# Optimization experiments

Measured on AMD Instinct MI355X. Metric: run time of the kernel, lower is better.

## Reference

```python
import jax, jax.numpy as jnp
import numpy as np

HEADS = 16
DIM_HEAD = 64
QUERY_DIM = 1024
INNER_DIM = HEADS * DIM_HEAD  # 1024
SCALE = DIM_HEAD ** (-0.5)


def setup_inputs() -> dict:
    key = jax.random.key(0)
    ks = jax.random.split(key, 6)
    B, S = 4, 2048
    hidden_states = jax.random.normal(ks[0], (B, S, QUERY_DIM), dtype=jnp.float32)
    # Linear weights stored as [in, out] for x @ W convention
    init = 1.0 / np.sqrt(QUERY_DIM)
    Wq = jax.random.uniform(ks[1], (QUERY_DIM, INNER_DIM), jnp.float32, -init, init)
    Wk = jax.random.uniform(ks[2], (QUERY_DIM, INNER_DIM), jnp.float32, -init, init)
    Wv = jax.random.uniform(ks[3], (QUERY_DIM, INNER_DIM), jnp.float32, -init, init)
    Wo = jax.random.uniform(ks[4], (INNER_DIM, QUERY_DIM), jnp.float32, -init, init)
    bo = jax.random.uniform(ks[5], (QUERY_DIM,), jnp.float32, -init, init)
    return {"hidden_states": hidden_states, "Wq": Wq, "Wk": Wk, "Wv": Wv, "Wo": Wo, "bo": bo}


def reference(hidden_states, Wq, Wk, Wv, Wo, bo):
    B, S, _ = hidden_states.shape
    # Projections
    q = hidden_states @ Wq  # [B,S,inner]
    k = hidden_states @ Wk
    v = hidden_states @ Wv
    # [B, H, S, D]
    q = q.reshape(B, S, HEADS, DIM_HEAD).transpose(0, 2, 1, 3)
    k = k.reshape(B, S, HEADS, DIM_HEAD).transpose(0, 2, 1, 3)
    v = v.reshape(B, S, HEADS, DIM_HEAD).transpose(0, 2, 1, 3)
    # Attention scores and softmax (scale after matmul, as in source)
    scores = jnp.einsum('bhqd,bhkd->bhqk', q, k) * SCALE
    attn = jax.nn.softmax(scores, axis=-1)
    out = jnp.einsum('bhqk,bhkd->bhqd', attn, v)  # [B,H,S,D]
    out = out.transpose(0, 2, 1, 3).reshape(B, S, INNER_DIM)
    return out @ Wo + bo
```

## Files before the change

kernel.cpp:

```cpp
#include <hip/hip_runtime.h>
#include <stdint.h>

typedef short v8s __attribute__((ext_vector_type(8)));
typedef float v4f __attribute__((ext_vector_type(4)));
typedef unsigned int u32;
typedef unsigned short us;

#define LOG2E 1.44269504088896340736f

__device__ __forceinline__ u32 f2u(float x) {
  union { float f; u32 u; } t; t.f = x; return t.u;
}

__device__ __forceinline__ unsigned short bfr(float x) {
  u32 u = f2u(x);
  u32 r = u + 0x7FFFu + ((u >> 16) & 1u);
  return (unsigned short)(r >> 16);
}

__device__ __forceinline__ u32 pk2(float a, float b) {
  return __builtin_amdgcn_perm(f2u(b) + 0x8000u, f2u(a) + 0x8000u, 0x07060302u);
}

__device__ __forceinline__ void async16(const void* g, void* l) {
  __builtin_amdgcn_global_load_lds(
      (const __attribute__((address_space(1))) u32*)g,
      (__attribute__((address_space(3))) u32*)l, 16, 0, 0);
}

#define MFMA_K32(A, B, C) __builtin_amdgcn_mfma_f32_16x16x32_bf16((A), (B), (C), 0, 0, 0)

__global__ void cast_h_kernel(const float4* __restrict__ in, ushort4* __restrict__ out, int n4) {
  int i = blockIdx.x * blockDim.x + threadIdx.x;
  if (i < n4) {
    float4 v = in[i];
    ushort4 o;
    o.x = bfr(v.x); o.y = bfr(v.y); o.z = bfr(v.z); o.w = bfr(v.w);
    out[i] = o;
  }
}

__global__ void transpose_cast4_kernel(const float* __restrict__ W0, const float* __restrict__ W1,
                                       const float* __restrict__ W2, const float* __restrict__ W3,
                                       us* __restrict__ O0, us* __restrict__ O1,
                                       us* __restrict__ O2, us* __restrict__ O3) {
  __shared__ float tile[32][33];
  const int z = blockIdx.z;
  const float* in = (z == 0) ? W0 : (z == 1) ? W1 : (z == 2) ? W2 : W3;
  us* out = (z == 0) ? O0 : (z == 1) ? O1 : (z == 2) ? O2 : O3;
  const float scale = (z == 0) ? 0.125f * LOG2E : 1.0f;
  const int N = 1024;
  int n0 = blockIdx.x * 32, k0 = blockIdx.y * 32;
  int tx = threadIdx.x, ty = threadIdx.y;
#pragma unroll
  for (int j = 0; j < 32; j += 8)
    tile[ty + j][tx] = in[(size_t)(k0 + ty + j) * N + n0 + tx];
  __syncthreads();
#pragma unroll
  for (int j = 0; j < 32; j += 8)
    out[(size_t)(n0 + ty + j) * 1024 + k0 + tx] = bfr(tile[tx][ty + j] * scale);
}

template <int MODE>
__global__ __launch_bounds__(512, 2)
void gemm3_kernel(const us* __restrict__ A, const us* __restrict__ Bt,
                  us* __restrict__ dQ, us* __restrict__ dK, us* __restrict__ dV,
                  float* __restrict__ outF, const float* __restrict__ bias) {
  __shared__ __align__(16) us sm[73728];
  us* const AsB = sm;
  us* const BsB = sm + 3 * 8192;

  const int tid = threadIdx.x;
  const int wid = tid >> 6;
  const int lane = tid & 63;
  const int quad = lane >> 4;
  const int l16 = lane & 15;
  const int tile_m = blockIdx.y * 128;
  const int tile_n = blockIdx.x * 256;
  const bool vpath = (MODE == 3) && (tile_n >= 2048);

  const int srow = tid >> 3;
  const int sc = tid & 7;
  const int scg = sc ^ (srow & 7);

  const us* const GA = A + (size_t)(tile_m + srow) * 1024 + scg * 8;
  const us* const GB = Bt + (size_t)(tile_n + srow) * 1024 + scg * 8;
  us* const LA = AsB + srow * 64 + sc * 8;
  us* const LB = BsB + srow * 64 + sc * 8;

  auto ISSUE = [&](int j, int b) {
    const us* ga = GA + j * 64;
    us* la = LA + b * 8192;
#pragma unroll
    for (int it = 0; it < 2; ++it)
      async16(ga + it * 64 * 1024, la + it * 64 * 64);
    const us* gb = GB + j * 64;
    us* lb = LB + b * 16384;
#pragma unroll
    for (int it = 0; it < 4; ++it)
      async16(gb + it * 64 * 1024, lb + it * 64 * 64);
  };

  v4f zero = {0.f, 0.f, 0.f, 0.f};
  v4f acc[4][4];
#pragma unroll
  for (int i = 0; i < 4; ++i)
#pragma unroll
    for (int j = 0; j < 4; ++j) acc[i][j] = zero;

  const int wm = (wid >> 2) * 64;
  const int wn = (wid & 3) * 64;

  ISSUE(0, 0);
  ISSUE(1, 1);

  int bt = 0;
#pragma unroll 1
  for (int t = 0; t < 16; ++t) {
    if (t < 15)
      asm volatile("s_waitcnt vmcnt(6)" ::: "memory");
    else
      asm volatile("s_waitcnt vmcnt(0)" ::: "memory");
    __builtin_amdgcn_s_barrier();
    asm volatile("" ::: "memory");

    if (t + 2 < 16) {
      int b2 = bt + 2;
      if (b2 >= 3) b2 -= 3;
      ISSUE(t + 2, b2);
    }

    const us* As = AsB + bt * 8192;
    const us* Bs = BsB + bt * 16384;
#pragma unroll
    for (int ks = 0; ks < 2; ++ks) {
      v8s a[4], b[4];
#pragma unroll
      for (int i = 0; i < 4; ++i) {
        int row = wm + i * 16 + l16;
        a[i] = *(const v8s*)&As[row * 64 + (((ks * 4 + quad) ^ (row & 7)) * 8)];
      }
#pragma unroll
      for (int j = 0; j < 4; ++j) {
        int row = wn + j * 16 + l16;
        b[j] = *(const v8s*)&Bs[row * 64 + (((ks * 4 + quad) ^ (row & 7)) * 8)];
      }
      __builtin_amdgcn_s_setprio(1);
      if (vpath) {
#pragma unroll
        for (int i = 0; i < 4; ++i)
#pragma unroll
          for (int j = 0; j < 4; ++j)
            acc[i][j] = MFMA_K32(a[i], b[j], acc[i][j]);
      } else {
#pragma unroll
        for (int i = 0; i < 4; ++i)
#pragma unroll
          for (int j = 0; j < 4; ++j)
            acc[i][j] = MFMA_K32(b[j], a[i], acc[i][j]);
      }
      __builtin_amdgcn_s_setprio(0);
    }
    if (++bt >= 3) bt = 0;
  }

  if (MODE == 2) {
#pragma unroll
    for (int i = 0; i < 4; ++i) {
      int row = tile_m + wm + i * 16 + l16;
#pragma unroll
      for (int j = 0; j < 4; ++j) {
        int col = tile_n + wn + j * 16 + quad * 4;
        float4 bv = *(const float4*)&bias[col];
        float4 o;
        o.x = acc[i][j][0] + bv.x; o.y = acc[i][j][1] + bv.y;
        o.z = acc[i][j][2] + bv.z; o.w = acc[i][j][3] + bv.w;
        *(float4*)&outF[(size_t)row * 1024 + col] = o;
      }
    }
  } else if (!vpath) {
    us* base = (tile_n < 1024) ? dQ : dK;
    const int coln = tile_n & 1023;
#pragma unroll
    for (int i = 0; i < 4; ++i) {
      int row = tile_m + wm + i * 16 + l16;
      int b_ = row >> 11, s_ = row & 2047;
#pragma unroll
      for (int j = 0; j < 4; ++j) {
        int col = coln + wn + j * 16 + quad * 4;
        int h = (col >> 6) & 15, d = col & 63;
        uint2 pk = make_uint2(pk2(acc[i][j][0], acc[i][j][1]), pk2(acc[i][j][2], acc[i][j][3]));
        *(uint2*)&base[((size_t)(b_ * 16 + h) * 2048 + s_) * 64 + d] = pk;
      }
    }
  } else {
    __syncthreads();
    const int vn = tile_n - 2048;
#pragma unroll
    for (int i = 0; i < 4; ++i) {
      int sp = wm + (i >> 1) * 32 + quad * 8 + (i & 1) * 4;
#pragma unroll
      for (int j = 0; j < 4; ++j) {
        int col = wn + j * 16 + l16;
        uint2 pk = make_uint2(pk2(acc[i][j][0], acc[i][j][1]), pk2(acc[i][j][2], acc[i][j][3]));
        *(uint2*)&sm[col * 132 + sp] = pk;
      }
    }
    __syncthreads();
    const int b_ = tile_m >> 11;
    const int sbase = tile_m & 2047;
#pragma unroll
    for (int it = 0; it < 8; ++it) {
      int u = it * 512 + tid;
      int col = u >> 4, sp = (u & 15) * 8;
      v8s val = *(const v8s*)&sm[col * 132 + sp];
      int colg = vn + col;
      int h = (colg >> 6) & 15, d = colg & 63;
      *(v8s*)&dV[((size_t)(b_ * 16 + h) * 64 + d) * 2048 + sbase + sp] = val;
    }
  }
}

__global__ __launch_bounds__(256, 2)
void flash_kernel(const us* __restrict__ Q, const us* __restrict__ K,
                  const us* __restrict__ Vt, us* __restrict__ O) {
  __shared__ __align__(16) us sm[16384];
  us* Ks = sm;
  us* Vts = sm + 8192;

  const int tid = threadIdx.x;
  const int wid = tid >> 6;
  const int lane = tid & 63;
  const int quad = lane >> 4;
  const int l16 = lane & 15;
  const int id = blockIdx.x;
  const int bh = id & 63;
  const int q0 = (id >> 6) * 256;
  const int wq = wid * 64;
  const us* Qp = Q + (size_t)bh * (2048 * 64);
  const us* Kp = K + (size_t)bh * (2048 * 64);
  const us* Vp = Vt + (size_t)bh * (64 * 2048);

  v8s qB[4][2];
#pragma unroll
  for (int mi = 0; mi < 4; ++mi)
#pragma unroll
    for (int ks = 0; ks < 2; ++ks)
      qB[mi][ks] = *(const v8s*)&Qp[(size_t)(q0 + wq + mi * 16 + l16) * 64 + ks * 32 + quad * 8];

  v4f zero = {0.f, 0.f, 0.f, 0.f};
  v4f o[4][4];
#pragma unroll
  for (int i = 0; i < 4; ++i)
#pragma unroll
    for (int mi = 0; mi < 4; ++mi) o[i][mi] = zero;
  v4f l_acc[4] = {zero, zero, zero, zero};
  const us one_bf = 0x3F80;
  const v8s ones = {(short)one_bf, (short)one_bf, (short)one_bf, (short)one_bf,
                    (short)one_bf, (short)one_bf, (short)one_bf, (short)one_bf};

  for (int kv0 = 0; kv0 < 2048; kv0 += 128) {
    __syncthreads();
    {
      int r0 = wid * 32 + (lane >> 3);
      int c = lane & 7;
#pragma unroll
      for (int it = 0; it < 4; ++it) {
        int rr = r0 + it * 8;
        int cg = c ^ (rr & 7);
        async16(Kp + (size_t)(kv0 + rr) * 64 + cg * 8, &Ks[rr * 64 + c * 8]);
      }
    }
    {
      int d0 = wid * 16 + (lane >> 4);
      int c = lane & 15;
#pragma unroll
      for (int it = 0; it < 4; ++it) {
        int dd = d0 + it * 4;
        int cg = c ^ (dd & 15);
        async16(Vp + (size_t)dd * 2048 + kv0 + cg * 8, &Vts[dd * 128 + c * 8]);
      }
    }
    __syncthreads();

#pragma unroll
    for (int hf = 0; hf < 2; ++hf) {
      v4f sT[4][4];
#pragma unroll
      for (int m = 0; m < 4; ++m)
#pragma unroll
        for (int mi = 0; mi < 4; ++mi) sT[m][mi] = zero;
#pragma unroll
      for (int ks = 0; ks < 2; ++ks) {
        v8s kA[4];
#pragma unroll
        for (int m = 0; m < 4; ++m) {
          int kvr = hf * 64 + m * 16 + l16;
          int cc = (ks * 4 + quad) ^ (l16 & 7);
          kA[m] = *(const v8s*)&Ks[kvr * 64 + cc * 8];
        }
        __builtin_amdgcn_s_setprio(1);
#pragma unroll
        for (int m = 0; m < 4; ++m)
#pragma unroll
          for (int mi = 0; mi < 4; ++mi)
            sT[m][mi] = MFMA_K32(kA[m], qB[mi][ks], sT[m][mi]);
        __builtin_amdgcn_s_setprio(0);
      }

#pragma unroll
      for (int cp = 0; cp < 2; ++cp) {
        v8s bp[4];
#pragma unroll
        for (int mi = 0; mi < 4; ++mi) {
          union { u32 w[4]; v8s s; } u;
#pragma unroll
          for (int dm = 0; dm < 2; ++dm) {
            int m = cp * 2 + dm;
            float p0 = __builtin_amdgcn_exp2f(sT[m][mi][0]);
            float p1 = __builtin_amdgcn_exp2f(sT[m][mi][1]);
            float p2 = __builtin_amdgcn_exp2f(sT[m][mi][2]);
            float p3 = __builtin_amdgcn_exp2f(sT[m][mi][3]);
            u.w[dm * 2] = pk2(p0, p1);
            u.w[dm * 2 + 1] = pk2(p2, p3);
          }
          bp[mi] = u.s;
          l_acc[mi] = MFMA_K32(ones, bp[mi], l_acc[mi]);
        }
        __builtin_amdgcn_s_setprio(1);
#pragma unroll
        for (int i = 0; i < 4; ++i) {
          int d = i * 16 + l16;
          int cc = (hf * 8 + cp * 4 + quad) ^ (d & 15);
          v8s vt = *(const v8s*)&Vts[d * 128 + cc * 8];
#pragma unroll
          for (int mi = 0; mi < 4; ++mi)
            o[i][mi] = MFMA_K32(vt, bp[mi], o[i][mi]);
        }
        __builtin_amdgcn_s_setprio(0);
      }
    }
  }

  float invl[4];
#pragma unroll
  for (int mi = 0; mi < 4; ++mi) invl[mi] = 1.0f / l_acc[mi][0];

  __syncthreads();
#pragma unroll
  for (int mi = 0; mi < 4; ++mi) {
    int q = wq + mi * 16 + l16;
#pragma unroll
    for (int i = 0; i < 4; ++i)
#pragma unroll
      for (int rp = 0; rp < 4; rp += 2) {
        int d = i * 16 + quad * 4 + rp;
        u32 pk = pk2(o[i][mi][rp] * invl[mi], o[i][mi][rp + 1] * invl[mi]);
        *(u32*)&sm[q * 64 + ((d >> 3) ^ (q & 7)) * 8 + (d & 7)] = pk;
      }
  }
  __syncthreads();
  const int b_ = bh >> 4, h_ = bh & 15;
#pragma unroll
  for (int it = 0; it < 8; ++it) {
    int u = it * 256 + tid;
    int row = u >> 3, ch = u & 7;
    v8s val = *(const v8s*)&sm[row * 64 + (ch ^ (row & 7)) * 8];
    *(v8s*)&O[((size_t)(b_ * 2048 + q0 + row)) * 1024 + h_ * 64 + ch * 8] = val;
  }
}

extern "C" void kernel_launch(void* const* d_in, const int* in_sizes, int n_in,
                              void* d_out, int out_size, void* d_ws, size_t ws_size,
                              hipStream_t stream) {
  const float* Hs = (const float*)d_in[0];
  const float* Wq = (const float*)d_in[1];
  const float* Wk = (const float*)d_in[2];
  const float* Wv = (const float*)d_in[3];
  const float* Wo = (const float*)d_in[4];
  const float* bo = (const float*)d_in[5];
  float* out = (float*)d_out;
  char* ws = (char*)d_ws;
  const size_t MiB = 1ull << 20;
  us* Hb  = (us*)(ws);
  us* Wqt = (us*)(ws + 16 * MiB);
  us* Wkt = (us*)(ws + 18 * MiB);
  us* Wvt = (us*)(ws + 20 * MiB);
  us* Wot = (us*)(ws + 22 * MiB);
  us* Qb  = (us*)(ws + 24 * MiB);
  us* Kb  = (us*)(ws + 40 * MiB);
  us* Vtb = (us*)(ws + 56 * MiB);
  us* Ob  = Hb;
  (void)Wkt; (void)Wvt;

  cast_h_kernel<<<8192, 256, 0, stream>>>((const float4*)Hs, (ushort4*)Hb, 2097152);
  transpose_cast4_kernel<<<dim3(32, 32, 4), dim3(32, 8), 0, stream>>>(Wq, Wk, Wv, Wo,
                                                                      Wqt, Wkt, Wvt, Wot);
  gemm3_kernel<3><<<dim3(12, 64), 512, 0, stream>>>(Hb, Wqt, Qb, Kb, Vtb, nullptr, nullptr);
  flash_kernel<<<512, 256, 0, stream>>>(Qb, Kb, Vtb, Ob);
  gemm3_kernel<2><<<dim3(4, 64), 512, 0, stream>>>(Ob, Wot, nullptr, nullptr, nullptr, out, bo);
}
```

Before: 251.2 us.

## Merge prologue kernels, add 256x256 QKV GEMM, drop flash setprio

Fuses the hidden-state cast and the weight transpose-cast into a single prologue launch, which saves one kernel launch. The generic QKV GEMM is replaced by a dedicated kernel with 256x256 tiles, double-buffered async loads and an interleaved fragment schedule, giving more operand reuse per tile. The V path now writes its transposed output through an LDS staging buffer. The s_setprio hints around the MFMA blocks in the flash attention kernel are also removed. The larger tile halves the number of QKV blocks (384), which may leave some CUs underfilled, and the higher register pressure could cost occupancy.

```diff
diff --git a/kernel.cpp b/kernel.cpp
--- a/kernel.cpp
+++ b/kernel.cpp
@@ -30,35 +30,219 @@
 
 #define MFMA_K32(A, B, C) __builtin_amdgcn_mfma_f32_16x16x32_bf16((A), (B), (C), 0, 0, 0)
 
-__global__ void cast_h_kernel(const float4* __restrict__ in, ushort4* __restrict__ out, int n4) {
-  int i = blockIdx.x * blockDim.x + threadIdx.x;
-  if (i < n4) {
-    float4 v = in[i];
+__global__ __launch_bounds__(256)
+void prologue_kernel(const float4* __restrict__ Hs, ushort4* __restrict__ Hb,
+                     const float* __restrict__ W0, const float* __restrict__ W1,
+                     const float* __restrict__ W2, const float* __restrict__ W3,
+                     us* __restrict__ O0, us* __restrict__ O1,
+                     us* __restrict__ O2, us* __restrict__ O3) {
+  __shared__ float tile[32][33];
+  const int bid = blockIdx.x;
+  if (bid < 8192) {
+    int i = bid * 256 + threadIdx.x;
+    float4 v = Hs[i];
     ushort4 o;
     o.x = bfr(v.x); o.y = bfr(v.y); o.z = bfr(v.z); o.w = bfr(v.w);
-    out[i] = o;
-  }
-}
-
-__global__ void transpose_cast4_kernel(const float* __restrict__ W0, const float* __restrict__ W1,
-                                       const float* __restrict__ W2, const float* __restrict__ W3,
-                                       us* __restrict__ O0, us* __restrict__ O1,
-                                       us* __restrict__ O2, us* __restrict__ O3) {
-  __shared__ float tile[32][33];
-  const int z = blockIdx.z;
-  const float* in = (z == 0) ? W0 : (z == 1) ? W1 : (z == 2) ? W2 : W3;
-  us* out = (z == 0) ? O0 : (z == 1) ? O1 : (z == 2) ? O2 : O3;
-  const float scale = (z == 0) ? 0.125f * LOG2E : 1.0f;
-  const int N = 1024;
-  int n0 = blockIdx.x * 32, k0 = blockIdx.y * 32;
-  int tx = threadIdx.x, ty = threadIdx.y;
-#pragma unroll
-  for (int j = 0; j < 32; j += 8)
-    tile[ty + j][tx] = in[(size_t)(k0 + ty + j) * N + n0 + tx];
-  __syncthreads();
-#pragma unroll
-  for (int j = 0; j < 32; j += 8)
-    out[(size_t)(n0 + ty + j) * 1024 + k0 + tx] = bfr(tile[tx][ty + j] * scale);
+    Hb[i] = o;
+  } else {
+    const int b = bid - 8192;
+    const int z = b >> 10;
+    const int ti = b & 1023;
+    const float* in = (z == 0) ? W0 : (z == 1) ? W1 : (z == 2) ? W2 : W3;
+    us* out = (z == 0) ? O0 : (z == 1) ? O1 : (z == 2) ? O2 : O3;
+    const float scale = (z == 0) ? 0.125f * LOG2E : 1.0f;
+    const int N = 1024;
+    int n0 = (ti & 31) * 32, k0 = (ti >> 5) * 32;
+    int tx = threadIdx.x & 31, ty = threadIdx.x >> 5;
+#pragma unroll
+    for (int j = 0; j < 32; j += 8)
+      tile[ty + j][tx] = in[(size_t)(k0 + ty + j) * N + n0 + tx];
+    __syncthreads();
+#pragma unroll
+    for (int j = 0; j < 32; j += 8)
+      out[(size_t)(n0 + ty + j) * 1024 + k0 + tx] = bfr(tile[tx][ty + j] * scale);
+  }
+}
+
+__global__ __launch_bounds__(512, 2)
+void gemm_qkv_kernel(const us* __restrict__ A, const us* __restrict__ Bt,
+                     us* __restrict__ dQ, us* __restrict__ dK, us* __restrict__ dV) {
+  __shared__ __align__(16) us sm[67584];
+
+  const int tid = threadIdx.x;
+  const int wid = tid >> 6;
+  const int lane = tid & 63;
+  const int quad = lane >> 4;
+  const int l16 = lane & 15;
+  const int tile_m = blockIdx.y * 256;
+  const int tile_n = blockIdx.x * 256;
+  const bool vpath = (tile_n >= 2048);
+
+  const int wm = (wid >> 2) * 128;
+  const int wn = (wid & 3) * 64;
+
+  const int srow = tid >> 3;
+  const int sc = tid & 7;
+  const int scg = sc ^ (srow & 7);
+
+  auto ISSUE_TILE = [&](int kt, int bsel) {
+    const int k0 = kt * 64;
+    const us* gA = A + (size_t)(tile_m + srow) * 1024 + k0 + scg * 8;
+    us* lA = sm + bsel * 16384 + srow * 64 + sc * 8;
+#pragma unroll
+    for (int h = 0; h < 4; ++h)
+      async16(gA + (size_t)(h * 64) * 1024, lA + h * 64 * 64);
+    const us* gB = Bt + (size_t)(tile_n + srow) * 1024 + k0 + scg * 8;
+    us* lB = sm + 32768 + bsel * 16384 + srow * 64 + sc * 8;
+#pragma unroll
+    for (int h = 0; h < 4; ++h)
+      async16(gB + (size_t)(h * 64) * 1024, lB + h * 64 * 64);
+  };
+
+  v4f zero = {0.f, 0.f, 0.f, 0.f};
+  v4f acc[8][4];
+#pragma unroll
+  for (int i = 0; i < 8; ++i)
+#pragma unroll
+    for (int j = 0; j < 4; ++j) acc[i][j] = zero;
+
+  ISSUE_TILE(0, 0);
+
+  int buf = 0;
+#pragma unroll 1
+  for (int t = 0; t < 16; ++t) {
+    if (t < 15) {
+      ISSUE_TILE(t + 1, buf ^ 1);
+      asm volatile("s_waitcnt vmcnt(8)" ::: "memory");
+    } else {
+      asm volatile("s_waitcnt vmcnt(0)" ::: "memory");
+    }
+    __builtin_amdgcn_s_barrier();
+    asm volatile("" ::: "memory");
+
+    const us* As = sm + buf * 16384;
+    const us* Bs = sm + 32768 + buf * 16384;
+    v8s aF[4][2], b01[2][2], b23[2][2];
+
+#pragma unroll
+    for (int i = 0; i < 4; ++i)
+#pragma unroll
+      for (int ks = 0; ks < 2; ++ks) {
+        int row = wm + i * 16 + l16;
+        aF[i][ks] = *(const v8s*)&As[row * 64 + (((ks * 4 + quad) ^ (row & 7)) * 8)];
+      }
+#pragma unroll
+    for (int j = 0; j < 2; ++j)
+#pragma unroll
+      for (int ks = 0; ks < 2; ++ks) {
+        int row = wn + j * 16 + l16;
+        b01[j][ks] = *(const v8s*)&Bs[row * 64 + (((ks * 4 + quad) ^ (row & 7)) * 8)];
+      }
+    __builtin_amdgcn_s_setprio(1);
+#pragma unroll
+    for (int i = 0; i < 4; ++i)
+#pragma unroll
+      for (int j = 0; j < 2; ++j)
+#pragma unroll
+        for (int ks = 0; ks < 2; ++ks)
+          acc[i][j] = vpath ? MFMA_K32(aF[i][ks], b01[j][ks], acc[i][j])
+                            : MFMA_K32(b01[j][ks], aF[i][ks], acc[i][j]);
+    __builtin_amdgcn_s_setprio(0);
+
+    __builtin_amdgcn_s_barrier();
+#pragma unroll
+    for (int j = 0; j < 2; ++j)
+#pragma unroll
+      for (int ks = 0; ks < 2; ++ks) {
+        int row = wn + (j + 2) * 16 + l16;
+        b23[j][ks] = *(const v8s*)&Bs[row * 64 + (((ks * 4 + quad) ^ (row & 7)) * 8)];
+      }
+    __builtin_amdgcn_s_setprio(1);
+#pragma unroll
+    for (int i = 0; i < 4; ++i)
+#pragma unroll
+      for (int j = 0; j < 2; ++j)
+#pragma unroll
+        for (int ks = 0; ks < 2; ++ks)
+          acc[i][j + 2] = vpath ? MFMA_K32(aF[i][ks], b23[j][ks], acc[i][j + 2])
+                                : MFMA_K32(b23[j][ks], aF[i][ks], acc[i][j + 2]);
+    __builtin_amdgcn_s_setprio(0);
+
+    __builtin_amdgcn_s_barrier();
+#pragma unroll
+    for (int i = 0; i < 4; ++i)
+#pragma unroll
+      for (int ks = 0; ks < 2; ++ks) {
+        int row = wm + (i + 4) * 16 + l16;
+        aF[i][ks] = *(const v8s*)&As[row * 64 + (((ks * 4 + quad) ^ (row & 7)) * 8)];
+      }
+    __builtin_amdgcn_s_setprio(1);
+#pragma unroll
+    for (int i = 0; i < 4; ++i)
+#pragma unroll
+      for (int j = 0; j < 2; ++j)
+#pragma unroll
+        for (int ks = 0; ks < 2; ++ks)
+          acc[i + 4][j + 2] = vpath ? MFMA_K32(aF[i][ks], b23[j][ks], acc[i + 4][j + 2])
+                                    : MFMA_K32(b23[j][ks], aF[i][ks], acc[i + 4][j + 2]);
+    __builtin_amdgcn_s_setprio(0);
+
+    __builtin_amdgcn_s_barrier();
+    __builtin_amdgcn_s_setprio(1);
+#pragma unroll
+    for (int i = 0; i < 4; ++i)
+#pragma unroll
+      for (int j = 0; j < 2; ++j)
+#pragma unroll
+        for (int ks = 0; ks < 2; ++ks)
+          acc[i + 4][j] = vpath ? MFMA_K32(aF[i][ks], b01[j][ks], acc[i + 4][j])
+                                : MFMA_K32(b01[j][ks], aF[i][ks], acc[i + 4][j]);
+    __builtin_amdgcn_s_setprio(0);
+
+    buf ^= 1;
+  }
+
+  if (!vpath) {
+    us* base = (tile_n < 1024) ? dQ : dK;
+    const int coln = tile_n & 1023;
+#pragma unroll
+    for (int i = 0; i < 8; ++i) {
+      int row = tile_m + wm + i * 16 + l16;
+      int b_ = row >> 11, s_ = row & 2047;
+#pragma unroll
+      for (int j = 0; j < 4; ++j) {
+        int col = coln + wn + j * 16 + quad * 4;
+        int h = (col >> 6) & 15, d = col & 63;
+        uint2 pk = make_uint2(pk2(acc[i][j][0], acc[i][j][1]), pk2(acc[i][j][2], acc[i][j][3]));
+        *(uint2*)&base[((size_t)(b_ * 16 + h) * 2048 + s_) * 64 + d] = pk;
+      }
+    }
+  } else {
+    __syncthreads();
+    const int vn = tile_n - 2048;
+#pragma unroll
+    for (int i = 0; i < 8; ++i) {
+      int sp = wm + (i >> 1) * 32 + quad * 8 + (i & 1) * 4;
+#pragma unroll
+      for (int j = 0; j < 4; ++j) {
+        int col = wn + j * 16 + l16;
+        uint2 pk = make_uint2(pk2(acc[i][j][0], acc[i][j][1]), pk2(acc[i][j][2], acc[i][j][3]));
+        *(uint2*)&sm[col * 264 + sp] = pk;
+      }
+    }
+    __syncthreads();
+    const int b_ = tile_m >> 11;
+    const int sbase = tile_m & 2047;
+#pragma unroll
+    for (int it = 0; it < 16; ++it) {
+      int u = it * 512 + tid;
+      int col = u >> 5, sp = (u & 31) * 8;
+      v8s val = *(const v8s*)&sm[col * 264 + sp];
+      int colg = vn + col;
+      int h = (colg >> 6) & 15, d = colg & 63;
+      *(v8s*)&dV[((size_t)(b_ * 16 + h) * 64 + d) * 2048 + sbase + sp] = val;
+    }
+  }
 }
 
 template <int MODE>
@@ -299,13 +483,11 @@
           int cc = (ks * 4 + quad) ^ (l16 & 7);
           kA[m] = *(const v8s*)&Ks[kvr * 64 + cc * 8];
         }
-        __builtin_amdgcn_s_setprio(1);
 #pragma unroll
         for (int m = 0; m < 4; ++m)
 #pragma unroll
           for (int mi = 0; mi < 4; ++mi)
             sT[m][mi] = MFMA_K32(kA[m], qB[mi][ks], sT[m][mi]);
-        __builtin_amdgcn_s_setprio(0);
       }
 
 #pragma unroll
@@ -327,7 +509,6 @@
           bp[mi] = u.s;
           l_acc[mi] = MFMA_K32(ones, bp[mi], l_acc[mi]);
         }
-        __builtin_amdgcn_s_setprio(1);
 #pragma unroll
         for (int i = 0; i < 4; ++i) {
           int d = i * 16 + l16;
@@ -337,7 +518,6 @@
           for (int mi = 0; mi < 4; ++mi)
             o[i][mi] = MFMA_K32(vt, bp[mi], o[i][mi]);
         }
-        __builtin_amdgcn_s_setprio(0);
       }
     }
   }
@@ -393,10 +573,9 @@
   us* Ob  = Hb;
   (void)Wkt; (void)Wvt;
 
-  cast_h_kernel<<<8192, 256, 0, stream>>>((const float4*)Hs, (ushort4*)Hb, 2097152);
-  transpose_cast4_kernel<<<dim3(32, 32, 4), dim3(32, 8), 0, stream>>>(Wq, Wk, Wv, Wo,
-                                                                      Wqt, Wkt, Wvt, Wot);
-  gemm3_kernel<3><<<dim3(12, 64), 512, 0, stream>>>(Hb, Wqt, Qb, Kb, Vtb, nullptr, nullptr);
+  prologue_kernel<<<12288, 256, 0, stream>>>((const float4*)Hs, (ushort4*)Hb,
+                                             Wq, Wk, Wv, Wo, Wqt, Wkt, Wvt, Wot);
+  gemm_qkv_kernel<<<dim3(12, 32), 512, 0, stream>>>(Hb, Wqt, Qb, Kb, Vtb);
   flash_kernel<<<512, 256, 0, stream>>>(Qb, Kb, Vtb, Ob);
   gemm3_kernel<2><<<dim3(4, 64), 512, 0, stream>>>(Ob, Wot, nullptr, nullptr, nullptr, out, bo);
 }
```

New measurement: 293.5 us. 16.8% more time.

## Merge prologue kernels, swizzle GEMM tile order per XCD, drop setprio in flash

Applied to the files above, without the earlier changes.

Fuses the hidden-state cast and the four weight transpose-casts into one launch, so there is one fewer kernel launch and its gap. Remaps GEMM workgroup IDs so that consecutive tiles land on the same XCD (8-way chiplet swizzle), aiming for better L2 reuse of A/B tiles. Removes the s_setprio bracketing around the MFMA sections in the flash attention kernel. The swizzle assumes the workgroup count divides evenly by 8, and dropping setprio may change how waves interleave on the matrix cores.

```diff
diff --git a/kernel.cpp b/kernel.cpp
--- a/kernel.cpp
+++ b/kernel.cpp
@@ -30,35 +30,38 @@
 
 #define MFMA_K32(A, B, C) __builtin_amdgcn_mfma_f32_16x16x32_bf16((A), (B), (C), 0, 0, 0)
 
-__global__ void cast_h_kernel(const float4* __restrict__ in, ushort4* __restrict__ out, int n4) {
-  int i = blockIdx.x * blockDim.x + threadIdx.x;
-  if (i < n4) {
-    float4 v = in[i];
+__global__ __launch_bounds__(256)
+void prologue_kernel(const float4* __restrict__ Hs, ushort4* __restrict__ Hb,
+                     const float* __restrict__ W0, const float* __restrict__ W1,
+                     const float* __restrict__ W2, const float* __restrict__ W3,
+                     us* __restrict__ O0, us* __restrict__ O1,
+                     us* __restrict__ O2, us* __restrict__ O3) {
+  __shared__ float tile[32][33];
+  const int bid = blockIdx.x;
+  if (bid < 8192) {
+    int i = bid * 256 + threadIdx.x;
+    float4 v = Hs[i];
     ushort4 o;
     o.x = bfr(v.x); o.y = bfr(v.y); o.z = bfr(v.z); o.w = bfr(v.w);
-    out[i] = o;
-  }
-}
-
-__global__ void transpose_cast4_kernel(const float* __restrict__ W0, const float* __restrict__ W1,
-                                       const float* __restrict__ W2, const float* __restrict__ W3,
-                                       us* __restrict__ O0, us* __restrict__ O1,
-                                       us* __restrict__ O2, us* __restrict__ O3) {
-  __shared__ float tile[32][33];
-  const int z = blockIdx.z;
-  const float* in = (z == 0) ? W0 : (z == 1) ? W1 : (z == 2) ? W2 : W3;
-  us* out = (z == 0) ? O0 : (z == 1) ? O1 : (z == 2) ? O2 : O3;
-  const float scale = (z == 0) ? 0.125f * LOG2E : 1.0f;
-  const int N = 1024;
-  int n0 = blockIdx.x * 32, k0 = blockIdx.y * 32;
-  int tx = threadIdx.x, ty = threadIdx.y;
-#pragma unroll
-  for (int j = 0; j < 32; j += 8)
-    tile[ty + j][tx] = in[(size_t)(k0 + ty + j) * N + n0 + tx];
-  __syncthreads();
-#pragma unroll
-  for (int j = 0; j < 32; j += 8)
-    out[(size_t)(n0 + ty + j) * 1024 + k0 + tx] = bfr(tile[tx][ty + j] * scale);
+    Hb[i] = o;
+  } else {
+    const int b = bid - 8192;
+    const int z = b >> 10;
+    const int ti = b & 1023;
+    const float* in = (z == 0) ? W0 : (z == 1) ? W1 : (z == 2) ? W2 : W3;
+    us* out = (z == 0) ? O0 : (z == 1) ? O1 : (z == 2) ? O2 : O3;
+    const float scale = (z == 0) ? 0.125f * LOG2E : 1.0f;
+    const int N = 1024;
+    int n0 = (ti & 31) * 32, k0 = (ti >> 5) * 32;
+    int tx = threadIdx.x & 31, ty = threadIdx.x >> 5;
+#pragma unroll
+    for (int j = 0; j < 32; j += 8)
+      tile[ty + j][tx] = in[(size_t)(k0 + ty + j) * N + n0 + tx];
+    __syncthreads();
+#pragma unroll
+    for (int j = 0; j < 32; j += 8)
+      out[(size_t)(n0 + ty + j) * 1024 + k0 + tx] = bfr(tile[tx][ty + j] * scale);
+  }
 }
 
 template <int MODE>
@@ -75,8 +78,14 @@
   const int lane = tid & 63;
   const int quad = lane >> 4;
   const int l16 = lane & 15;
-  const int tile_m = blockIdx.y * 128;
-  const int tile_n = blockIdx.x * 256;
+
+  const int gdx = gridDim.x;
+  const int nwg = gdx * gridDim.y;
+  const int cpx = nwg >> 3;
+  const int id0 = blockIdx.y * gdx + blockIdx.x;
+  const int swz = (id0 & 7) * cpx + (id0 >> 3);
+  const int tile_m = (swz / gdx) * 128;
+  const int tile_n = (swz % gdx) * 256;
   const bool vpath = (MODE == 3) && (tile_n >= 2048);
 
   const int srow = tid >> 3;
@@ -299,13 +308,11 @@
           int cc = (ks * 4 + quad) ^ (l16 & 7);
           kA[m] = *(const v8s*)&Ks[kvr * 64 + cc * 8];
         }
-        __builtin_amdgcn_s_setprio(1);
 #pragma unroll
         for (int m = 0; m < 4; ++m)
 #pragma unroll
           for (int mi = 0; mi < 4; ++mi)
             sT[m][mi] = MFMA_K32(kA[m], qB[mi][ks], sT[m][mi]);
-        __builtin_amdgcn_s_setprio(0);
       }
 
 #pragma unroll
@@ -327,7 +334,6 @@
           bp[mi] = u.s;
           l_acc[mi] = MFMA_K32(ones, bp[mi], l_acc[mi]);
         }
-        __builtin_amdgcn_s_setprio(1);
 #pragma unroll
         for (int i = 0; i < 4; ++i) {
           int d = i * 16 + l16;
@@ -337,7 +343,6 @@
           for (int mi = 0; mi < 4; ++mi)
             o[i][mi] = MFMA_K32(vt, bp[mi], o[i][mi]);
         }
-        __builtin_amdgcn_s_setprio(0);
       }
     }
   }
@@ -393,9 +398,8 @@
   us* Ob  = Hb;
   (void)Wkt; (void)Wvt;
 
-  cast_h_kernel<<<8192, 256, 0, stream>>>((const float4*)Hs, (ushort4*)Hb, 2097152);
-  transpose_cast4_kernel<<<dim3(32, 32, 4), dim3(32, 8), 0, stream>>>(Wq, Wk, Wv, Wo,
-                                                                      Wqt, Wkt, Wvt, Wot);
+  prologue_kernel<<<12288, 256, 0, stream>>>((const float4*)Hs, (ushort4*)Hb,
+                                             Wq, Wk, Wv, Wo, Wqt, Wkt, Wvt, Wot);
   gemm3_kernel<3><<<dim3(12, 64), 512, 0, stream>>>(Hb, Wqt, Qb, Kb, Vtb, nullptr, nullptr);
   flash_kernel<<<512, 256, 0, stream>>>(Qb, Kb, Vtb, Ob);
   gemm3_kernel<2><<<dim3(4, 64), 512, 0, stream>>>(Ob, Wot, nullptr, nullptr, nullptr, out, bo);
```

Measured after the change: 263.1 us. 4.7% more time.
